# Kernel tuning notes

Hardware: AMD Instinct MI355X
Metric: run time of the kernel (lower is better)

## Reference

```python
import jax, jax.numpy as jnp
import numpy as np
import math

B, C, T0, Q0 = 2, 48, 250, 65
H = 192; KS = 4; HS = 1; NH = 4; E = 8; F = 65; DV = 12; HID2 = 384
EPS = 1e-5


def ln_clamp(x, g, b, axes, eps=EPS):
    # LayerNormalization4D / 4DCF: std = sqrt(clamp(var, eps))
    mu = x.mean(axis=axes, keepdims=True)
    var = x.var(axis=axes, keepdims=True)
    return (x - mu) / jnp.sqrt(jnp.maximum(var, eps)) * g + b


def torch_ln(x, g, b, eps=EPS):
    # torch.nn.LayerNorm over last dim: sqrt(var + eps)
    mu = x.mean(axis=-1, keepdims=True)
    var = x.var(axis=-1, keepdims=True)
    return (x - mu) / jnp.sqrt(var + eps) * g + b


def mha(x, in_w, in_b, out_w, out_b, nh):
    # torch.nn.MultiheadAttention, batch_first, self-attention
    N, L, Cm = x.shape
    qkv = x @ in_w.T + in_b
    q, k, v = jnp.split(qkv, 3, axis=-1)
    dh = Cm // nh
    hd = lambda t: t.reshape(N, L, nh, dh).transpose(0, 2, 1, 3)
    q, k, v = hd(q), hd(k), hd(v)
    att = jax.nn.softmax(jnp.einsum('nhld,nhmd->nhlm', q, k) / jnp.sqrt(jnp.float32(dh)), axis=-1)
    o = jnp.einsum('nhlm,nhmd->nhld', att, v).transpose(0, 2, 1, 3).reshape(N, L, Cm)
    return o @ out_w.T + out_b


def lstm_dir(x, wi, wh, bi, bh, reverse=False):
    # x: [N, L, D]; torch gate order i,f,g,o
    Hd = wh.shape[1]
    xs = jnp.swapaxes(x, 0, 1)
    if reverse:
        xs = xs[::-1]
    pre = jnp.einsum('lnd,gd->lng', xs, wi) + bi + bh  # [L,N,4H]

    def step(carry, p):
        hprev, cprev = carry
        gates = p + hprev @ wh.T
        i, f, g, o = jnp.split(gates, 4, axis=-1)
        c = jax.nn.sigmoid(f) * cprev + jax.nn.sigmoid(i) * jnp.tanh(g)
        hnew = jax.nn.sigmoid(o) * jnp.tanh(c)
        return (hnew, c), hnew

    h0 = jnp.zeros((x.shape[0], Hd), x.dtype)
    _, ys = jax.lax.scan(step, (h0, h0), pre)
    if reverse:
        ys = ys[::-1]
    return jnp.swapaxes(ys, 0, 1)


def bilstm(x, wif, whf, bif, bhf, wib, whb, bib, bhb):
    return jnp.concatenate([lstm_dir(x, wif, whf, bif, bhf, False),
                            lstm_dir(x, wib, whb, bib, bhb, True)], axis=-1)


def unfold1d(x, ks, hs):
    # x: [N, C, Q] -> [N, L, C*ks], channel-major like F.unfold
    N, Cc, Qq = x.shape
    L = (Qq - ks) // hs + 1
    cols = jnp.stack([x[:, :, k:k + (L - 1) * hs + 1:hs] for k in range(ks)], axis=-1)  # [N,C,L,ks]
    return cols.transpose(0, 2, 1, 3).reshape(N, L, Cc * ks)


def conv_transpose1d(x, w, b, stride):
    # x: [N, Cin, L], w: [Cin, Cout, ks] (torch ConvTranspose1d layout); overlap-add
    N, Ci, L = x.shape
    ks = w.shape[2]
    out_len = (L - 1) * stride + ks
    y = jnp.einsum('nil,iok->nolk', x, w)
    out = jnp.zeros((N, w.shape[1], out_len), x.dtype)
    for k in range(ks):
        out = out.at[:, :, k:k + (L - 1) * stride + 1:stride].add(y[..., k])
    return out + b[:, None]


def _forward(x, af_in_w, af_in_b, af_out_w, af_out_b, naf_g, naf_b, at_in_w, at_in_b, at_out_w, at_out_b, nat_g, nat_b, intra_ng, intra_nb, inter_ng, inter_nb, intra_wif, intra_whf, intra_bif, intra_bhf, intra_wib, intra_whb, intra_bib, intra_bhb, inter_wif, inter_whf, inter_bif, inter_bhf, inter_wib, inter_whb, inter_bib, inter_bhb, il_w, il_b, itl_w, itl_b, qw, qb, qa, qg, qbt, kw, kb, ka, kg, kbt, vw, vb, va, vg, vbt, pw, pb, pa, pg, pbt, fin_w, fin_b, fdw_w, fdw_b, fout_w, fout_b):
    Bb, Cc, old_T, old_Q = x.shape
    T = math.ceil((old_T - KS) / HS) * HS + KS
    Qd = math.ceil((old_Q - KS) / HS) * HS + KS
    x = jnp.pad(x, ((0, 0), (0, 0), (0, T - old_T), (0, Qd - old_Q)))
    input_ = x

    # ---- intra (frequency) path ----
    z = ln_clamp(input_, intra_ng[None, :, None, None], intra_nb[None, :, None, None], (1,))
    seq = z.transpose(0, 2, 3, 1).reshape(Bb * T, Qd, Cc)  # [B*T, Q, C]
    att = mha(seq, af_in_w, af_in_b, af_out_w, af_out_b, NH)
    seq = torch_ln(att + seq, naf_g, naf_b)
    u = unfold1d(seq.transpose(0, 2, 1), KS, HS)
    r = bilstm(u, intra_wif, intra_whf, intra_bif, intra_bhf, intra_wib, intra_whb, intra_bib, intra_bhb)
    r = conv_transpose1d(r.transpose(0, 2, 1), il_w, il_b, HS)  # [B*T, C, Qd]
    intra = r.reshape(Bb, T, Cc, Qd).transpose(0, 2, 1, 3) + input_
    input_ = intra

    # ---- inter (time) path ----
    z = ln_clamp(input_, inter_ng[None, :, None, None], inter_nb[None, :, None, None], (1,))
    seq = z.transpose(0, 3, 2, 1).reshape(Bb * Qd, T, Cc)  # [B*Q, T, C]
    att = mha(seq, at_in_w, at_in_b, at_out_w, at_out_b, NH)
    seq = torch_ln(att + seq, nat_g, nat_b)
    u = unfold1d(seq.transpose(0, 2, 1), KS, HS)
    r = bilstm(u, inter_wif, inter_whf, inter_bif, inter_bhf, inter_wib, inter_whb, inter_bib, inter_bhb)
    r = conv_transpose1d(r.transpose(0, 2, 1), itl_w, itl_b, HS)  # [B*Qd, C, T]
    inter = r.reshape(Bb, Qd, Cc, T).transpose(0, 2, 3, 1) + input_
    inter = inter[:, :, :old_T, :old_Q]

    # ---- custom per-head conv attention ----
    bt = inter  # [B, C, t, f]

    def head_proj(w, bias, a, g, beta):
        y = jnp.einsum('bctf,hec->hbetf', bt, w) + bias[:, None, :, None, None]
        y = jnp.where(y >= 0, y, a[:, None, None, None, None] * y)  # PReLU per head
        return ln_clamp(y, g[:, None, :, None, :], beta[:, None, :, None, :], (2, 4))

    Qh = head_proj(qw, qb, qa, qg, qbt)  # [h,B,E,t,f]
    Kh = head_proj(kw, kb, ka, kg, kbt)
    Vh = head_proj(vw, vb, va, vg, vbt)  # [h,B,dv,t,f]
    h_, _, E_, t_, f_ = Qh.shape
    dv = Vh.shape[2]
    Qf = Qh.transpose(0, 1, 3, 2, 4).reshape(h_, Bb, t_, E_ * f_)
    Kf = Kh.transpose(0, 1, 3, 2, 4).reshape(h_, Bb, t_, E_ * f_)
    Vf = Vh.transpose(0, 1, 3, 2, 4).reshape(h_, Bb, t_, dv * f_)
    attm = jax.nn.softmax(jnp.einsum('hbtd,hbsd->hbts', Qf, Kf) / jnp.sqrt(jnp.float32(E_ * f_)), axis=-1)
    Vo = jnp.einsum('hbts,hbsd->hbtd', attm, Vf).reshape(h_, Bb, t_, dv, f_)
    Vo = Vo.transpose(1, 0, 3, 2, 4).reshape(Bb, h_ * dv, t_, f_)  # head-major channel concat
    pj = jnp.einsum('bctf,oc->botf', Vo, pw) + pb[None, :, None, None]
    pj = jnp.where(pj >= 0, pj, pa * pj)
    pj = ln_clamp(pj, pg[None, :, None, :], pbt[None, :, None, :], (1, 3))
    out = pj + inter

    # ---- gated-dconv FFN ----
    pi = jnp.einsum('bctf,oc->botf', out, fin_w) + fin_b[None, :, None, None]
    dwc = jax.lax.conv_general_dilated(pi, fdw_w, (1, 1), ((1, 1), (1, 1)),
                                       dimension_numbers=('NCHW', 'OIHW', 'NCHW'),
                                       feature_group_count=fdw_w.shape[0]) + fdw_b[None, :, None, None]
    x1, x2 = jnp.split(dwc, 2, axis=1)
    ffn = jnp.einsum('bctf,oc->botf', jax.nn.gelu(x1, approximate=False) * x2, fout_w) + fout_b[None, :, None, None]
    return ffn + out


def setup_inputs() -> dict:
    key = jax.random.key(0)
    cnt = [0]

    def rn(shape, s=0.05):
        cnt[0] += 1
        return jax.random.normal(jax.random.fold_in(key, cnt[0]), shape, dtype=jnp.float32) * s

    z = lambda *s: jnp.zeros(s, jnp.float32)
    o = lambda *s: jnp.ones(s, jnp.float32)
    d = {}
    d['x'] = rn((B, C, T0, Q0), 1.0)
    for p in ['af', 'at']:
        d[p + '_in_w'] = rn((3 * C, C)); d[p + '_in_b'] = z(3 * C)
        d[p + '_out_w'] = rn((C, C)); d[p + '_out_b'] = z(C)
    d['naf_g'] = o(C); d['naf_b'] = z(C); d['nat_g'] = o(C); d['nat_b'] = z(C)
    d['intra_ng'] = o(C); d['intra_nb'] = z(C); d['inter_ng'] = o(C); d['inter_nb'] = z(C)
    for p in ['intra', 'inter']:
        for s in ['f', 'b']:
            d[p + '_wi' + s] = rn((4 * H, C * KS)); d[p + '_wh' + s] = rn((4 * H, H))
            d[p + '_bi' + s] = z(4 * H); d[p + '_bh' + s] = z(4 * H)
    d['il_w'] = rn((2 * H, C, KS)); d['il_b'] = z(C)
    d['itl_w'] = rn((2 * H, C, KS)); d['itl_b'] = z(C)
    for p, dim in [('q', E), ('k', E), ('v', DV)]:
        d[p + 'w'] = rn((NH, dim, C)); d[p + 'b'] = z(NH, dim)
        d[p + 'a'] = 0.25 * o(NH); d[p + 'g'] = o(NH, dim, F); d[p + 'bt'] = z(NH, dim, F)
    d['pw'] = rn((C, C)); d['pb'] = z(C); d['pa'] = 0.25 * o(1); d['pg'] = o(C, F); d['pbt'] = z(C, F)
    d['fin_w'] = rn((HID2, C)); d['fin_b'] = z(HID2)
    d['fdw_w'] = rn((HID2, 1, 3, 3)); d['fdw_b'] = z(HID2)
    d['fout_w'] = rn((C, HID2 // 2)); d['fout_b'] = z(C)
    return d


def reference(x, af_in_w, af_in_b, af_out_w, af_out_b, naf_g, naf_b, at_in_w, at_in_b, at_out_w, at_out_b, nat_g, nat_b, intra_ng, intra_nb, inter_ng, inter_nb, intra_wif, intra_whf, intra_bif, intra_bhf, intra_wib, intra_whb, intra_bib, intra_bhb, inter_wif, inter_whf, inter_bif, inter_bhf, inter_wib, inter_whb, inter_bib, inter_bhb, il_w, il_b, itl_w, itl_b, qw, qb, qa, qg, qbt, kw, kb, ka, kg, kbt, vw, vb, va, vg, vbt, pw, pb, pa, pg, pbt, fin_w, fin_b, fdw_w, fdw_b, fout_w, fout_b):
    return _forward(x, af_in_w, af_in_b, af_out_w, af_out_b, naf_g, naf_b, at_in_w, at_in_b, at_out_w, at_out_b, nat_g, nat_b, intra_ng, intra_nb, inter_ng, inter_nb, intra_wif, intra_whf, intra_bif, intra_bhf, intra_wib, intra_whb, intra_bib, intra_bhb, inter_wif, inter_whf, inter_bif, inter_bhf, inter_wib, inter_whb, inter_bib, inter_bhb, il_w, il_b, itl_w, itl_b, qw, qb, qa, qg, qbt, kw, kb, ka, kg, kbt, vw, vb, va, vg, vbt, pw, pb, pa, pg, pbt, fin_w, fin_b, fdw_w, fdw_b, fout_w, fout_b)
```

## Files before the change

### kernel.cpp

```cpp
#include <hip/hip_runtime.h>
#include <math.h>

#define EPSV 1e-5f

typedef _Float16 v2h __attribute__((ext_vector_type(2)));

__device__ __forceinline__ float sigf(float x){ return 1.0f/(1.0f+__expf(-x)); }
__device__ __forceinline__ float tanhf_(float x){
  float c = fminf(fmaxf(x,-10.f),10.f);
  float e = __expf(2.0f*c);
  return (e-1.0f)/(e+1.0f);
}

__device__ __forceinline__ void ldsbar(){
  asm volatile("s_waitcnt lgkmcnt(0)\n\ts_barrier" ::: "memory");
}

__device__ __forceinline__ float dot2u(unsigned int a, unsigned int b, float c){
#if __has_builtin(__builtin_amdgcn_fdot2)
  v2h av = __builtin_bit_cast(v2h, a);
  v2h bv = __builtin_bit_cast(v2h, b);
  return __builtin_amdgcn_fdot2(av, bv, c, false);
#else
  v2h av = __builtin_bit_cast(v2h, a);
  v2h bv = __builtin_bit_cast(v2h, b);
  return c + (float)av.x*(float)bv.x + (float)av.y*(float)bv.y;
#endif
}

__global__ void k_ln_chan(const float* __restrict__ src, float* __restrict__ dst,
                          const float* __restrict__ g, const float* __restrict__ bb, int mode){
  int i = blockIdx.x*blockDim.x + threadIdx.x;
  const int total = 2*250*65;
  if (i >= total) return;
  int q = i % 65; int t = (i/65) % 250; int b = i/(65*250);
  const float* p = src + (size_t)b*48*250*65 + (size_t)t*65 + q;
  float s=0.f, ss=0.f;
  for (int c=0;c<48;c++){ float v = p[(size_t)c*250*65]; s+=v; ss+=v*v; }
  float mu = s*(1.0f/48.0f);
  float var = ss*(1.0f/48.0f) - mu*mu;
  float rs = rsqrtf(fmaxf(var, EPSV));
  float* d = (mode==0) ? dst + ((size_t)(b*250+t)*65 + q)*48
                       : dst + ((size_t)(b*65+q)*250 + t)*48;
  for (int c=0;c<48;c++){ float v = p[(size_t)c*250*65]; d[c] = (v-mu)*rs*g[c] + bb[c]; }
}

__global__ __launch_bounds__(256) void k_mha2(
    const float* __restrict__ seq, const float* __restrict__ inw,
    const float* __restrict__ inb, float* __restrict__ att, int N, int L){
  __shared__ float shq[250*12];
  __shared__ float shk[250*12];
  __shared__ float shv[250*12];
  int n = blockIdx.x, h = blockIdx.y;
  for (int i = threadIdx.x; i < L*36; i += 256){
    int l = i/36, jj = i - (i/36)*36;
    int sect = jj/12, d = jj - sect*12;
    int j = sect*48 + h*12 + d;
    const float* srow = seq + ((size_t)n*L + l)*48;
    const float* wrow = inw + j*48;
    float acc = inb[j];
    for (int c=0;c<48;c++) acc += srow[c]*wrow[c];
    float* dst = (sect==0)?shq:(sect==1)?shk:shv;
    dst[l*12+d] = acc;
  }
  __syncthreads();
  const float scale = 0.28867513459481287f;
  for (int r = threadIdx.x; r < L; r += 256){
    const float4* q4 = (const float4*)(shq + r*12);
    float4 q0 = q4[0], q1 = q4[1], q2 = q4[2];
    float m = -1e30f, den = 0.0f;
    float4 o0 = make_float4(0,0,0,0), o1 = make_float4(0,0,0,0), o2 = make_float4(0,0,0,0);
    for (int j=0; j<L; j++){
      const float4* k4 = (const float4*)(shk + j*12);
      float4 k0 = k4[0], k1 = k4[1], k2 = k4[2];
      float s = q0.x*k0.x + q0.y*k0.y + q0.z*k0.z + q0.w*k0.w
              + q1.x*k1.x + q1.y*k1.y + q1.z*k1.z + q1.w*k1.w
              + q2.x*k2.x + q2.y*k2.y + q2.z*k2.z + q2.w*k2.w;
      s *= scale;
      if (s > m){
        float corr = __expf(m - s);
        den *= corr;
        o0.x*=corr; o0.y*=corr; o0.z*=corr; o0.w*=corr;
        o1.x*=corr; o1.y*=corr; o1.z*=corr; o1.w*=corr;
        o2.x*=corr; o2.y*=corr; o2.z*=corr; o2.w*=corr;
        m = s;
      }
      float e = __expf(s - m);
      den += e;
      const float4* v4 = (const float4*)(shv + j*12);
      float4 v0 = v4[0], v1 = v4[1], v2 = v4[2];
      o0.x += e*v0.x; o0.y += e*v0.y; o0.z += e*v0.z; o0.w += e*v0.w;
      o1.x += e*v1.x; o1.y += e*v1.y; o1.z += e*v1.z; o1.w += e*v1.w;
      o2.x += e*v2.x; o2.y += e*v2.y; o2.z += e*v2.z; o2.w += e*v2.w;
    }
    float inv = 1.0f/den;
    float* outp = att + ((size_t)n*L + r)*48 + h*12;
    outp[0]=o0.x*inv; outp[1]=o0.y*inv; outp[2]=o0.z*inv; outp[3]=o0.w*inv;
    outp[4]=o1.x*inv; outp[5]=o1.y*inv; outp[6]=o1.z*inv; outp[7]=o1.w*inv;
    outp[8]=o2.x*inv; outp[9]=o2.y*inv; outp[10]=o2.z*inv; outp[11]=o2.w*inv;
  }
}

__global__ void k_projres(const float* __restrict__ att, const float* __restrict__ seq,
                          const float* __restrict__ w, const float* __restrict__ bias,
                          float* __restrict__ dst, int NL){
  int i = blockIdx.x*blockDim.x + threadIdx.x;
  if (i >= NL*48) return;
  int o = i % 48; int nl = i/48;
  const float* ar = att + (size_t)nl*48;
  const float* wr = w + o*48;
  float acc = bias[o] + seq[i];
  for (int c=0;c<48;c++) acc += ar[c]*wr[c];
  dst[i] = acc;
}

__global__ void k_rowln(float* __restrict__ buf, const float* __restrict__ g,
                        const float* __restrict__ bb, int NL){
  int nl = blockIdx.x*blockDim.x + threadIdx.x;
  if (nl >= NL) return;
  float* p = buf + (size_t)nl*48;
  float s=0.f, ss=0.f;
  for (int c=0;c<48;c++){ float v=p[c]; s+=v; ss+=v*v; }
  float mu = s*(1.0f/48.0f);
  float var = ss*(1.0f/48.0f) - mu*mu;
  float rs = rsqrtf(var + EPSV);
  for (int c=0;c<48;c++) p[c] = (p[c]-mu)*rs*g[c] + bb[c];
}

__global__ void k_prep(const float* __restrict__ s0, const float* __restrict__ s1,
                       const float* __restrict__ s2, const float* __restrict__ s3,
                       const float* __restrict__ s4, const float* __restrict__ s5,
                       const float* __restrict__ s6, const float* __restrict__ s7,
                       const float* __restrict__ c0, const float* __restrict__ c1,
                       unsigned int* __restrict__ wpk, unsigned int* __restrict__ wtp){
  int i = blockIdx.x*blockDim.x + threadIdx.x;
  if (i < 589824){
    int seg = i/73728, off = i - seg*73728;
    const float* w = (seg==0)?s0:(seg==1)?s1:(seg==2)?s2:(seg==3)?s3:(seg==4)?s4:(seg==5)?s5:(seg==6)?s6:s7;
    int g = off % 768, d2 = off / 768;
    v2h v; v.x = (_Float16)w[g*192 + 2*d2]; v.y = (_Float16)w[g*192 + 2*d2 + 1];
    wpk[(size_t)seg*73728 + (size_t)d2*768 + g] = __builtin_bit_cast(unsigned int, v);
  } else if (i < 589824 + 2*36864){
    int j = i - 589824;
    int seg = j/36864, off = j - seg*36864;
    const float* w = seg ? c1 : c0;
    int c = off % 48; int ii2 = (off/48) % 192; int k = off/(48*192);
    v2h v;
    v.x = (_Float16)w[(2*ii2)*192 + c*4 + k];
    v.y = (_Float16)w[(2*ii2+1)*192 + c*4 + k];
    wtp[(size_t)seg*36864 + off] = __builtin_bit_cast(unsigned int, v);
  }
}

__global__ __launch_bounds__(256) void k_pregates(
    const float* __restrict__ seq2, const unsigned int* __restrict__ wi,
    const float* __restrict__ bi, const float* __restrict__ bh,
    _Float16* __restrict__ pre, int L2, int SL){
  __shared__ unsigned int ut[96*16];
  int n = blockIdx.y;
  int l0 = blockIdx.x*16;
  int t = threadIdx.x;
  for (int idx=t; idx<1536; idx+=256){
    int l = idx & 15, d2 = idx >> 4;
    int li = l0 + l;
    int c = d2 >> 1, k0 = (d2 & 1)*2;
    float u0=0.f, u1=0.f;
    if (li < L2){
      const float* p = seq2 + ((size_t)n*SL + li)*48;
      u0 = p[k0*48 + c];
      u1 = p[(k0+1)*48 + c];
    }
    v2h v; v.x=(_Float16)u0; v.y=(_Float16)u1;
    ut[d2*16 + l] = __builtin_bit_cast(unsigned int, v);
  }
  __syncthreads();
  float acc[3][16];
  float b0 = bi[t] + bh[t];
  float b1 = bi[t+256] + bh[t+256];
  float b2 = bi[t+512] + bh[t+512];
  #pragma unroll
  for (int l=0;l<16;l++){ acc[0][l]=b0; acc[1][l]=b1; acc[2][l]=b2; }
  #pragma unroll 4
  for (int d2=0; d2<96; d2++){
    unsigned int w0 = wi[(size_t)d2*768 + t];
    unsigned int w1 = wi[(size_t)d2*768 + t + 256];
    unsigned int w2 = wi[(size_t)d2*768 + t + 512];
    const uint4* u4 = (const uint4*)(ut + d2*16);
    #pragma unroll
    for (int l4=0; l4<4; l4++){
      uint4 uu = u4[l4];
      acc[0][l4*4+0] = dot2u(uu.x, w0, acc[0][l4*4+0]);
      acc[0][l4*4+1] = dot2u(uu.y, w0, acc[0][l4*4+1]);
      acc[0][l4*4+2] = dot2u(uu.z, w0, acc[0][l4*4+2]);
      acc[0][l4*4+3] = dot2u(uu.w, w0, acc[0][l4*4+3]);
      acc[1][l4*4+0] = dot2u(uu.x, w1, acc[1][l4*4+0]);
      acc[1][l4*4+1] = dot2u(uu.y, w1, acc[1][l4*4+1]);
      acc[1][l4*4+2] = dot2u(uu.z, w1, acc[1][l4*4+2]);
      acc[1][l4*4+3] = dot2u(uu.w, w1, acc[1][l4*4+3]);
      acc[2][l4*4+0] = dot2u(uu.x, w2, acc[2][l4*4+0]);
      acc[2][l4*4+1] = dot2u(uu.y, w2, acc[2][l4*4+1]);
      acc[2][l4*4+2] = dot2u(uu.z, w2, acc[2][l4*4+2]);
      acc[2][l4*4+3] = dot2u(uu.w, w2, acc[2][l4*4+3]);
    }
  }
  #pragma unroll
  for (int l=0;l<16;l++){
    int li = l0 + l;
    if (li < L2){
      _Float16* pr = pre + ((size_t)n*L2 + li)*768;
      pr[t]       = (_Float16)acc[0][l];
      pr[t+256]   = (_Float16)acc[1][l];
      pr[t+512]   = (_Float16)acc[2][l];
    }
  }
}

template<int G>
__global__ __launch_bounds__(1024) void k_lstm6(
    const _Float16* __restrict__ pre, unsigned int* __restrict__ rT2,
    const unsigned int* __restrict__ wh_f, const unsigned int* __restrict__ wh_b,
    int N, int L2){
  __shared__ unsigned int hh2[96*G];
  __shared__ float gpart[4*G*768];
  _Float16* hh2h = (_Float16*)hh2;
  int t = threadIdx.x;
  int q = t >> 8, tt = t & 255;
  int dir = blockIdx.y;
  int n0 = blockIdx.x*G;
  const unsigned int* wh = dir ? wh_b : wh_f;
  unsigned int wq[24][3];
  #pragma unroll
  for (int i=0;i<24;i++){
    const unsigned int* wr = wh + (size_t)(q*24+i)*768 + tt;
    wq[i][0] = wr[0]; wq[i][1] = wr[256]; wq[i][2] = wr[512];
  }
  const _Float16* prd = pre + (size_t)dir*(size_t)N*L2*768;
  float cst = 0.f;
  int as = t/192, aj = t - as*192;
  bool actv = (t < 192*G);
  const unsigned short* pbase = (const unsigned short*)prd;
  if (actv) pbase = (const unsigned short*)(prd + ((size_t)(n0+as)*L2)*768) + aj;
  for (int idx=t; idx<96*G; idx+=1024) hh2[idx]=0u;
  __syncthreads();

  unsigned short c0=0,c1=0,c2=0,c3=0;
  {
    int l0 = dir ? (L2-1) : 0;
    if (actv){
      const unsigned short* pp = pbase + (size_t)l0*768;
      c0 = pp[0]; c1 = pp[192]; c2 = pp[384]; c3 = pp[576];
    }
  }

  for (int step=0; step<L2; step++){
    int l = dir ? (L2-1-step) : step;
    int stepn = (step+1 < L2) ? (step+1) : step;
    int ln = dir ? (L2-1-stepn) : stepn;
    unsigned short pn0=0,pn1=0,pn2=0,pn3=0;
    if (actv){
      const unsigned short* pp = pbase + (size_t)ln*768;
      pn0 = pp[0]; pn1 = pp[192]; pn2 = pp[384]; pn3 = pp[576];
    }

    float acc0[G], acc1[G], acc2[G];
    #pragma unroll
    for (int s=0;s<G;s++){ acc0[s]=0.f; acc1[s]=0.f; acc2[s]=0.f; }
    #pragma unroll
    for (int i=0;i<24;i++){
      unsigned int hhv[G];
      if (G==4){
        uint4 hv = ((const uint4*)hh2)[q*24+i];
        hhv[0]=hv.x; hhv[1]=hv.y; hhv[2]=hv.z; hhv[3]=hv.w;
      } else if (G==2){
        uint2 hv = ((const uint2*)hh2)[q*24+i];
        hhv[0]=hv.x; hhv[1]=hv.y;
      } else {
        hhv[0] = hh2[q*24+i];
      }
      unsigned int w0 = wq[i][0], w1 = wq[i][1], w2 = wq[i][2];
      #pragma unroll
      for (int s=0;s<G;s++){
        acc0[s] = dot2u(hhv[s], w0, acc0[s]);
        acc1[s] = dot2u(hhv[s], w1, acc1[s]);
        acc2[s] = dot2u(hhv[s], w2, acc2[s]);
      }
    }
    #pragma unroll
    for (int s=0;s<G;s++){
      gpart[(q*G+s)*768 + tt]       = acc0[s];
      gpart[(q*G+s)*768 + tt + 256] = acc1[s];
      gpart[(q*G+s)*768 + tt + 512] = acc2[s];
    }
    ldsbar();

    if (actv){
      float gi = (float)__builtin_bit_cast(_Float16, c0);
      float gf = (float)__builtin_bit_cast(_Float16, c1);
      float gg = (float)__builtin_bit_cast(_Float16, c2);
      float go = (float)__builtin_bit_cast(_Float16, c3);
      #pragma unroll
      for (int qq=0; qq<4; qq++){
        const float* gp = gpart + (qq*G+as)*768;
        gi += gp[aj]; gf += gp[aj+192]; gg += gp[aj+384]; go += gp[aj+576];
      }
      float ig = sigf(gi), fg = sigf(gf), g2 = tanhf_(gg), og = sigf(go);
      cst = fg*cst + ig*g2;
      float hn = og*tanhf_(cst);
      hh2h[((aj>>1)*G + as)*2 + (aj&1)] = (_Float16)hn;
    }
    ldsbar();

    if (t < 96*G){
      int s = t/96, ii2 = t - s*96;
      unsigned int v = hh2[ii2*G + s];
      rT2[((size_t)(n0+s)*192 + dir*96 + ii2)*L2 + l] = v;
    }
    c0 = pn0; c1 = pn1; c2 = pn2; c3 = pn3;
  }
}

__global__ __launch_bounds__(256) void k_convt4(
    const unsigned int* __restrict__ rT2, const unsigned int* __restrict__ wtp,
    const float* __restrict__ bias, const float* __restrict__ resid,
    float* __restrict__ dst, int L2, int OL, int mode){
  int n = blockIdx.y;
  int pos = blockIdx.x*64 + (threadIdx.x & 63);
  int cq = __builtin_amdgcn_readfirstlane((int)(threadIdx.x >> 6));
  float acc[12];
  #pragma unroll
  for (int c=0;c<12;c++) acc[c]=0.f;
  const unsigned int* rbase = rT2 + (size_t)n*192*L2;
  for (int k=0;k<4;k++){
    int l = pos - k;
    bool v = (l>=0) && (l<L2);
    int lc = v ? l : 0;
    const unsigned int* wk = wtp + (size_t)k*192*48 + cq*12;
    #pragma unroll 4
    for (int ii2=0; ii2<192; ii2++){
      unsigned int rp = v ? rbase[(size_t)ii2*L2 + lc] : 0u;
      const unsigned int* wrow = wk + ii2*48;
      #pragma unroll
      for (int c=0;c<12;c++) acc[c] = dot2u(rp, wrow[c], acc[c]);
    }
  }
  if (pos < OL){
    for (int c12=0;c12<12;c12++){
      int c = cq*12 + c12;
      size_t oidx;
      if (mode==0){ int b=n/250, t=n%250; oidx = (((size_t)b*48+c)*250+t)*65+pos; }
      else        { int b=n/65,  qq=n%65; oidx = (((size_t)b*48+c)*250+pos)*65+qq; }
      dst[oidx] = acc[c12] + bias[c] + resid[oidx];
    }
  }
}

__global__ __launch_bounds__(256) void k_hproj(
    const float* __restrict__ bt, const float* __restrict__ w,
    const float* __restrict__ bias, const float* __restrict__ alpha,
    const float* __restrict__ g, const float* __restrict__ beta,
    float* __restrict__ dst, int dim, int kt_mode){
  __shared__ float tsh[3120];
  __shared__ float ybuf[780];
  __shared__ float r1[256];
  __shared__ float r2[256];
  int bx = blockIdx.x;
  int h = bx/500; int rem = bx - h*500; int b = rem/250; int t = rem - b*250;
  int ny = dim*65;
  int tid = threadIdx.x;
  const float* bbase = bt + (size_t)b*48*250*65 + (size_t)t*65;
  for (int kidx=tid; kidx<3120; kidx+=256){
    int c = kidx/65, f = kidx - c*65;
    tsh[kidx] = bbase[(size_t)c*250*65 + f];
  }
  __syncthreads();
  float al = alpha[h];
  float s=0.f, ss=0.f;
  for (int kidx=tid; kidx<ny; kidx+=256){
    int e = kidx/65, f = kidx - e*65;
    const float* wr = w + (h*dim+e)*48;
    float acc = bias[h*dim+e];
    for (int c=0;c<48;c++) acc += tsh[c*65+f]*wr[c];
    if (acc < 0.f) acc *= al;
    ybuf[kidx] = acc; s += acc; ss += acc*acc;
  }
  r1[tid]=s; r2[tid]=ss; __syncthreads();
  for (int st=128; st>0; st>>=1){
    if (tid<st){ r1[tid]+=r1[tid+st]; r2[tid]+=r2[tid+st]; }
    __syncthreads();
  }
  float mu = r1[0]/(float)ny, var = r2[0]/(float)ny - mu*mu;
  float rs = rsqrtf(fmaxf(var, EPSV));
  for (int kidx=tid; kidx<ny; kidx+=256){
    float y = (ybuf[kidx]-mu)*rs*g[h*ny+kidx] + beta[h*ny+kidx];
    if (kt_mode) dst[((size_t)(h*2+b)*520 + kidx)*250 + t] = y;
    else         dst[(size_t)bx*ny + kidx] = y;
  }
}

__global__ __launch_bounds__(256) void k_headattn2(
    const float* __restrict__ Qp, const float* __restrict__ KT,
    const float* __restrict__ Vp, float* __restrict__ Vo){
  __shared__ float qsh[10*520];
  __shared__ float psh[10*250];
  __shared__ float rinv[10];
  int t0 = blockIdx.x*10;
  int hb = blockIdx.y;
  int h = hb >> 1, b = hb & 1;
  int tid = threadIdx.x;
  const float* qbase = Qp + ((size_t)hb*250 + t0)*520;
  for (int i=tid; i<5200; i+=256) qsh[i] = qbase[i];
  __syncthreads();
  const float scale = 0.04385290096535147f;
  if (tid < 250){
    float sc[10];
    #pragma unroll
    for (int i=0;i<10;i++) sc[i]=0.f;
    const float* kcol = KT + (size_t)hb*520*250 + tid;
    for (int d=0; d<520; d++){
      float kv = kcol[(size_t)d*250];
      #pragma unroll
      for (int i=0;i<10;i++) sc[i] += qsh[i*520+d]*kv;
    }
    #pragma unroll
    for (int i=0;i<10;i++) psh[i*250+tid] = sc[i]*scale;
  }
  __syncthreads();
  if (tid < 10){
    float m = -1e30f;
    for (int s2=0;s2<250;s2++) m = fmaxf(m, psh[tid*250+s2]);
    float den = 0.f;
    for (int s2=0;s2<250;s2++){
      float e = __expf(psh[tid*250+s2]-m);
      psh[tid*250+s2]=e; den+=e;
    }
    rinv[tid] = 1.0f/den;
  }
  __syncthreads();
  float acc[10][4];
  #pragma unroll
  for (int i=0;i<10;i++)
    #pragma unroll
    for (int s=0;s<4;s++) acc[i][s]=0.f;
  for (int s2=0; s2<250; s2++){
    const float* vrow = Vp + ((size_t)hb*250 + s2)*780;
    float p[10];
    #pragma unroll
    for (int i=0;i<10;i++) p[i] = psh[i*250+s2];
    #pragma unroll
    for (int slot=0; slot<4; slot++){
      int d = tid + slot*256;
      if (d < 780){
        float v = vrow[d];
        #pragma unroll
        for (int i=0;i<10;i++) acc[i][slot] += p[i]*v;
      }
    }
  }
  #pragma unroll
  for (int slot=0; slot<4; slot++){
    int d = tid + slot*256;
    if (d < 780){
      int e = d/65, f = d - e*65;
      #pragma unroll
      for (int i=0;i<10;i++){
        Vo[(((size_t)b*48 + h*12 + e)*250 + (t0+i))*65 + f] = acc[i][slot]*rinv[i];
      }
    }
  }
}

__global__ __launch_bounds__(256) void k_pprojln(
    const float* __restrict__ Vo, const float* __restrict__ pw,
    const float* __restrict__ pb, const float* __restrict__ pa,
    const float* __restrict__ pg, const float* __restrict__ pbt,
    const float* __restrict__ inter, float* __restrict__ outb){
  __shared__ float vsh[3120];
  __shared__ float ysh[3120];
  __shared__ float r1[256];
  __shared__ float r2[256];
  int bx = blockIdx.x;
  int t = bx % 250, b = bx/250;
  int tid = threadIdx.x;
  const float* vbase = Vo + (size_t)b*48*250*65 + (size_t)t*65;
  for (int k=tid; k<3120; k+=256){
    int c = k/65, f = k - c*65;
    vsh[k] = vbase[(size_t)c*250*65 + f];
  }
  __syncthreads();
  float pav = pa[0];
  float s=0.f, ss=0.f;
  for (int k=tid; k<3120; k+=256){
    int o = k/65, f = k - o*65;
    const float* wr = pw + o*48;
    float acc = pb[o];
    for (int c=0;c<48;c++) acc += vsh[c*65+f]*wr[c];
    if (acc < 0.f) acc *= pav;
    ysh[k] = acc; s += acc; ss += acc*acc;
  }
  r1[tid]=s; r2[tid]=ss; __syncthreads();
  for (int st=128; st>0; st>>=1){
    if (tid<st){ r1[tid]+=r1[tid+st]; r2[tid]+=r2[tid+st]; }
    __syncthreads();
  }
  float mu = r1[0]*(1.0f/3120.0f), var = r2[0]*(1.0f/3120.0f) - mu*mu;
  float rs = rsqrtf(fmaxf(var, EPSV));
  for (int k=tid; k<3120; k+=256){
    int c = k/65, f = k - c*65;
    size_t idx = (((size_t)b*48+c)*250 + t)*65 + f;
    outb[idx] = (ysh[k]-mu)*rs*pg[k] + pbt[k] + inter[idx];
  }
}

__global__ void k_fin2(const float* __restrict__ outb, const float* __restrict__ w,
                       const float* __restrict__ bias, float* __restrict__ pi){
  int i = blockIdx.x*blockDim.x + threadIdx.x;
  if (i >= 2*96*250*65) return;
  int f = i % 65;
  int t = (i/65) % 250;
  int og = (i/(65*250)) % 96;
  int b = i/(65*250*96);
  const float* xp = outb + (size_t)b*48*250*65 + (size_t)t*65 + f;
  const float* w0 = w + og*4*48;
  float a0=bias[og*4], a1=bias[og*4+1], a2=bias[og*4+2], a3=bias[og*4+3];
  for (int c=0;c<48;c++){
    float xv = xp[(size_t)c*250*65];
    a0 += xv*w0[c]; a1 += xv*w0[48+c]; a2 += xv*w0[96+c]; a3 += xv*w0[144+c];
  }
  size_t o0 = (((size_t)b*384 + og*4)*250 + t)*65 + f;
  pi[o0] = a0; pi[o0+16250] = a1; pi[o0+2*16250] = a2; pi[o0+3*16250] = a3;
}

__global__ void k_dwg(const float* __restrict__ pi, const float* __restrict__ dw,
                      const float* __restrict__ db, float* __restrict__ gbuf){
  int i = blockIdx.x*blockDim.x + threadIdx.x;
  if (i >= 2*192*250*65) return;
  int f = i % 65;
  int t = (i/65) % 250;
  int j = (i/(65*250)) % 192;
  int b = i/(65*250*192);
  float x12[2];
  for (int half=0; half<2; half++){
    int ch = j + half*192;
    const float* base = pi + ((size_t)b*384 + ch)*250*65;
    const float* wr = dw + ch*9;
    float acc = db[ch];
    for (int dt=-1; dt<=1; dt++){
      int tt = t+dt;
      if (tt<0||tt>=250) continue;
      for (int df=-1; df<=1; df++){
        int ff = f+df;
        if (ff<0||ff>=65) continue;
        acc += base[(size_t)tt*65+ff]*wr[(dt+1)*3 + (df+1)];
      }
    }
    x12[half]=acc;
  }
  float x1 = x12[0];
  float g = 0.5f*x1*(1.0f+erff(x1*0.70710678118654752f));
  gbuf[i] = g * x12[1];
}

__global__ void k_final2(const float* __restrict__ gbuf, const float* __restrict__ w,
                         const float* __restrict__ bias, const float* __restrict__ outb,
                         float* __restrict__ dout){
  int i = blockIdx.x*blockDim.x + threadIdx.x;
  if (i >= 2*12*250*65) return;
  int f = i % 65;
  int t = (i/65) % 250;
  int og = (i/(65*250)) % 12;
  int b = i/(65*250*12);
  const float* gp = gbuf + (size_t)b*192*250*65 + (size_t)t*65 + f;
  const float* w0 = w + og*4*192;
  float a0=bias[og*4], a1=bias[og*4+1], a2=bias[og*4+2], a3=bias[og*4+3];
  for (int j=0;j<192;j++){
    float gv = gp[(size_t)j*250*65];
    a0 += gv*w0[j]; a1 += gv*w0[192+j]; a2 += gv*w0[384+j]; a3 += gv*w0[576+j];
  }
  size_t o0 = (((size_t)b*48 + og*4)*250 + t)*65 + f;
  dout[o0]         = a0 + outb[o0];
  dout[o0+16250]   = a1 + outb[o0+16250];
  dout[o0+2*16250] = a2 + outb[o0+2*16250];
  dout[o0+3*16250] = a3 + outb[o0+3*16250];
}

extern "C" void kernel_launch(void* const* d_in, const int* in_sizes, int n_in,
                              void* d_out, int out_size, void* d_ws, size_t ws_size,
                              hipStream_t stream) {
  (void)in_sizes; (void)n_in; (void)out_size; (void)ws_size;
  auto in = [&](int i){ return (const float*)d_in[i]; };
  const float* x        = in(0);
  const float* af_in_w  = in(1);  const float* af_in_b  = in(2);
  const float* af_out_w = in(3);  const float* af_out_b = in(4);
  const float* at_in_w  = in(5);  const float* at_in_b  = in(6);
  const float* at_out_w = in(7);  const float* at_out_b = in(8);
  const float* naf_g = in(9),  *naf_b = in(10), *nat_g = in(11), *nat_b = in(12);
  const float* intra_ng = in(13), *intra_nb = in(14), *inter_ng = in(15), *inter_nb = in(16);
  const float* intra_wif = in(17), *intra_whf = in(18), *intra_bif = in(19), *intra_bhf = in(20);
  const float* intra_wib = in(21), *intra_whb = in(22), *intra_bib = in(23), *intra_bhb = in(24);
  const float* inter_wif = in(25), *inter_whf = in(26), *inter_bif = in(27), *inter_bhf = in(28);
  const float* inter_wib = in(29), *inter_whb = in(30), *inter_bib = in(31), *inter_bhb = in(32);
  const float* il_w = in(33), *il_b = in(34), *itl_w = in(35), *itl_b = in(36);
  const float* qw = in(37), *qb = in(38), *qa = in(39), *qg = in(40), *qbt = in(41);
  const float* kw = in(42), *kb = in(43), *ka = in(44), *kg = in(45), *kbt = in(46);
  const float* vw = in(47), *vb = in(48), *va = in(49), *vg = in(50), *vbt = in(51);
  const float* pw = in(52), *pb = in(53), *pa = in(54), *pg = in(55), *pbt = in(56);
  const float* fin_w = in(57), *fin_b = in(58), *fdw_w = in(59), *fdw_b = in(60);
  const float* fout_w = in(61), *fout_b = in(62);

  float* ws = (float*)d_ws;
  float* buf_intra = ws + 0;
  float* buf_bt    = ws + 1560000;
  float* buf_out   = ws + 3120000;
  unsigned int* wpk = (unsigned int*)(ws + 4680000);
  unsigned int* wtp = (unsigned int*)(ws + 5269824);
  float* scr       = ws + 5343552;
  float* s_seq2 = scr;
  float* s_seq  = scr + 1560000;
  float* s_att  = scr + 3120000;
  _Float16* s_pre = (_Float16*)(scr + 4680000);
  unsigned int* s_rT2 = (unsigned int*)(scr + 29340480);
  float* s_Qh = scr;
  float* s_KT = scr + 1040000;
  float* s_Vh = scr + 2080000;
  float* s_Vo = scr + 3640000;
  float* s_pi = scr;
  float* s_g  = scr + 12480000;

  const int thr = 256;
  auto cdiv = [](int a, int b){ return (a+b-1)/b; };

  k_prep<<<cdiv(663552,thr),thr,0,stream>>>(
      intra_wif, intra_whf, intra_wib, intra_whb,
      inter_wif, inter_whf, inter_wib, inter_whb,
      il_w, itl_w, wpk, wtp);

  k_ln_chan<<<cdiv(2*250*65,thr), thr, 0, stream>>>(x, s_seq, intra_ng, intra_nb, 0);
  k_mha2<<<dim3(500,4), 256, 0, stream>>>(s_seq, af_in_w, af_in_b, s_att, 500, 65);
  k_projres<<<cdiv(500*65*48,thr), thr, 0, stream>>>(s_att, s_seq, af_out_w, af_out_b, s_seq2, 500*65);
  k_rowln<<<cdiv(32500,thr), thr, 0, stream>>>(s_seq2, naf_g, naf_b, 32500);
  {
    const size_t dstr = (size_t)500*62*768;
    k_pregates<<<dim3(4,500), 256, 0, stream>>>(s_seq2, wpk+0*73728, intra_bif, intra_bhf, s_pre,        62, 65);
    k_pregates<<<dim3(4,500), 256, 0, stream>>>(s_seq2, wpk+2*73728, intra_bib, intra_bhb, s_pre + dstr, 62, 65);
  }
  k_lstm6<2><<<dim3(250,2), 1024, 0, stream>>>(s_pre, s_rT2, wpk+1*73728, wpk+3*73728, 500, 62);
  k_convt4<<<dim3(2,500), 256, 0, stream>>>(s_rT2, wtp+0*36864, il_b, x, buf_intra, 62, 65, 0);

  k_ln_chan<<<cdiv(2*250*65,thr),thr,0,stream>>>(buf_intra, s_seq, inter_ng, inter_nb, 1);
  k_mha2<<<dim3(130,4), 256, 0, stream>>>(s_seq, at_in_w, at_in_b, s_att, 130, 250);
  k_projres<<<cdiv(130*250*48,thr),thr,0,stream>>>(s_att, s_seq, at_out_w, at_out_b, s_seq2, 130*250);
  k_rowln<<<cdiv(32500,thr),thr,0,stream>>>(s_seq2, nat_g, nat_b, 32500);
  {
    const size_t dstr = (size_t)130*247*768;
    k_pregates<<<dim3(16,130), 256, 0, stream>>>(s_seq2, wpk+4*73728, inter_bif, inter_bhf, s_pre,        247, 250);
    k_pregates<<<dim3(16,130), 256, 0, stream>>>(s_seq2, wpk+6*73728, inter_bib, inter_bhb, s_pre + dstr, 247, 250);
  }
  k_lstm6<1><<<dim3(130,2), 1024, 0, stream>>>(s_pre, s_rT2, wpk+5*73728, wpk+7*73728, 130, 247);
  k_convt4<<<dim3(4,130), 256, 0, stream>>>(s_rT2, wtp+1*36864, itl_b, buf_intra, buf_bt, 247, 250, 1);

  k_hproj<<<2000,256,0,stream>>>(buf_bt, qw, qb, qa, qg, qbt, s_Qh, 8, 0);
  k_hproj<<<2000,256,0,stream>>>(buf_bt, kw, kb, ka, kg, kbt, s_KT, 8, 1);
  k_hproj<<<2000,256,0,stream>>>(buf_bt, vw, vb, va, vg, vbt, s_Vh, 12, 0);
  k_headattn2<<<dim3(25,8), 256, 0, stream>>>(s_Qh, s_KT, s_Vh, s_Vo);
  k_pprojln<<<500,256,0,stream>>>(s_Vo, pw, pb, pa, pg, pbt, buf_bt, buf_out);

  k_fin2<<<cdiv(2*96*250*65,thr),thr,0,stream>>>(buf_out, fin_w, fin_b, s_pi);
  k_dwg<<<cdiv(2*192*250*65,thr),thr,0,stream>>>(s_pi, fdw_w, fdw_b, s_g);
  k_final2<<<cdiv(2*12*250*65,thr),thr,0,stream>>>(s_g, fout_w, fout_b, buf_out, (float*)d_out);
}
```

Baseline: 2.542 ms.

## Split LSTM recurrent weights between transposed LDS copy and global streaming

The recurrent LSTM kernel drops from 1024 to 512 threads per block. The first half of the hidden-weight matrix is copied into LDS once, transposed, so each thread can read contiguous uint4 chunks. The other half is reloaded from global memory on every time step. This removes the large per-thread register weight cache and halves the partial-sum buffer and its reduction, aiming to cut register pressure and barrier cost. The trade-off is global or L2 weight traffic inside the serial time loop, a large LDS footprint, and half the threads doing the dot products.

```diff
diff --git a/kernel.cpp b/kernel.cpp
--- a/kernel.cpp
+++ b/kernel.cpp
@@ -216,31 +216,32 @@
 }
 
 template<int G>
-__global__ __launch_bounds__(1024) void k_lstm6(
+__global__ __launch_bounds__(512,1) void k_lstm11(
     const _Float16* __restrict__ pre, unsigned int* __restrict__ rT2,
     const unsigned int* __restrict__ wh_f, const unsigned int* __restrict__ wh_b,
     int N, int L2){
+  __shared__ unsigned int wshT[48*768];
   __shared__ unsigned int hh2[96*G];
-  __shared__ float gpart[4*G*768];
+  __shared__ float gpart[2*G*768];
   _Float16* hh2h = (_Float16*)hh2;
   int t = threadIdx.x;
-  int q = t >> 8, tt = t & 255;
+  int hf = t >> 8, tt = t & 255;
   int dir = blockIdx.y;
   int n0 = blockIdx.x*G;
   const unsigned int* wh = dir ? wh_b : wh_f;
-  unsigned int wq[24][3];
-  #pragma unroll
-  for (int i=0;i<24;i++){
-    const unsigned int* wr = wh + (size_t)(q*24+i)*768 + tt;
-    wq[i][0] = wr[0]; wq[i][1] = wr[256]; wq[i][2] = wr[512];
-  }
+
+  for (int idx=t; idx<48*768; idx+=512){
+    int d2 = idx/768, row = idx - d2*768;
+    wshT[row*48 + d2] = wh[idx];
+  }
+  for (int idx=t; idx<96*G; idx+=512) hh2[idx]=0u;
+
   const _Float16* prd = pre + (size_t)dir*(size_t)N*L2*768;
   float cst = 0.f;
   int as = t/192, aj = t - as*192;
   bool actv = (t < 192*G);
   const unsigned short* pbase = (const unsigned short*)prd;
   if (actv) pbase = (const unsigned short*)(prd + ((size_t)(n0+as)*L2)*768) + aj;
-  for (int idx=t; idx<96*G; idx+=1024) hh2[idx]=0u;
   __syncthreads();
 
   unsigned short c0=0,c1=0,c2=0,c3=0;
@@ -251,6 +252,8 @@
       c0 = pp[0]; c1 = pp[192]; c2 = pp[384]; c3 = pp[576];
     }
   }
+
+  const unsigned int* wstr = wh + 48*768 + tt;
 
   for (int step=0; step<L2; step++){
     int l = dir ? (L2-1-step) : step;
@@ -265,31 +268,62 @@
     float acc0[G], acc1[G], acc2[G];
     #pragma unroll
     for (int s=0;s<G;s++){ acc0[s]=0.f; acc1[s]=0.f; acc2[s]=0.f; }
-    #pragma unroll
-    for (int i=0;i<24;i++){
-      unsigned int hhv[G];
-      if (G==4){
-        uint4 hv = ((const uint4*)hh2)[q*24+i];
-        hhv[0]=hv.x; hhv[1]=hv.y; hhv[2]=hv.z; hhv[3]=hv.w;
-      } else if (G==2){
-        uint2 hv = ((const uint2*)hh2)[q*24+i];
-        hhv[0]=hv.x; hhv[1]=hv.y;
-      } else {
-        hhv[0] = hh2[q*24+i];
+
+    if (hf==0){
+      const uint4* w0p = (const uint4*)(wshT + (size_t)tt*48);
+      const uint4* w1p = (const uint4*)(wshT + (size_t)(tt+256)*48);
+      const uint4* w2p = (const uint4*)(wshT + (size_t)(tt+512)*48);
+      #pragma unroll 4
+      for (int blk=0; blk<12; blk++){
+        unsigned int hw[4][G];
+        if (G==1){
+          uint4 hv = ((const uint4*)hh2)[blk];
+          hw[0][0]=hv.x; hw[1][0]=hv.y; hw[2][0]=hv.z; hw[3][0]=hv.w;
+        } else {
+          uint4 ha = ((const uint4*)hh2)[blk*2];
+          uint4 hb = ((const uint4*)hh2)[blk*2+1];
+          hw[0][0]=ha.x; hw[0][1]=ha.y; hw[1][0]=ha.z; hw[1][1]=ha.w;
+          hw[2][0]=hb.x; hw[2][1]=hb.y; hw[3][0]=hb.z; hw[3][1]=hb.w;
+        }
+        uint4 w0 = w0p[blk], w1 = w1p[blk], w2 = w2p[blk];
+        const unsigned int* w0a = (const unsigned int*)&w0;
+        const unsigned int* w1a = (const unsigned int*)&w1;
+        const unsigned int* w2a = (const unsigned int*)&w2;
+        #pragma unroll
+        for (int j=0;j<4;j++){
+          #pragma unroll
+          for (int s=0;s<G;s++){
+            acc0[s] = dot2u(hw[j][s], w0a[j], acc0[s]);
+            acc1[s] = dot2u(hw[j][s], w1a[j], acc1[s]);
+            acc2[s] = dot2u(hw[j][s], w2a[j], acc2[s]);
+          }
+        }
       }
-      unsigned int w0 = wq[i][0], w1 = wq[i][1], w2 = wq[i][2];
-      #pragma unroll
-      for (int s=0;s<G;s++){
-        acc0[s] = dot2u(hhv[s], w0, acc0[s]);
-        acc1[s] = dot2u(hhv[s], w1, acc1[s]);
-        acc2[s] = dot2u(hhv[s], w2, acc2[s]);
+    } else {
+      #pragma unroll 8
+      for (int i=0;i<48;i++){
+        unsigned int h2v[G];
+        if (G==1){ h2v[0] = hh2[48+i]; }
+        else {
+          uint2 hv = *(const uint2*)&hh2[(48+i)*2];
+          h2v[0]=hv.x; h2v[1]=hv.y;
+        }
+        unsigned int w0 = wstr[(size_t)i*768];
+        unsigned int w1 = wstr[(size_t)i*768 + 256];
+        unsigned int w2 = wstr[(size_t)i*768 + 512];
+        #pragma unroll
+        for (int s=0;s<G;s++){
+          acc0[s] = dot2u(h2v[s], w0, acc0[s]);
+          acc1[s] = dot2u(h2v[s], w1, acc1[s]);
+          acc2[s] = dot2u(h2v[s], w2, acc2[s]);
+        }
       }
     }
     #pragma unroll
     for (int s=0;s<G;s++){
-      gpart[(q*G+s)*768 + tt]       = acc0[s];
-      gpart[(q*G+s)*768 + tt + 256] = acc1[s];
-      gpart[(q*G+s)*768 + tt + 512] = acc2[s];
+      gpart[(hf*G+s)*768 + tt]       = acc0[s];
+      gpart[(hf*G+s)*768 + tt + 256] = acc1[s];
+      gpart[(hf*G+s)*768 + tt + 512] = acc2[s];
     }
     ldsbar();
 
@@ -299,8 +333,8 @@
       float gg = (float)__builtin_bit_cast(_Float16, c2);
       float go = (float)__builtin_bit_cast(_Float16, c3);
       #pragma unroll
-      for (int qq=0; qq<4; qq++){
-        const float* gp = gpart + (qq*G+as)*768;
+      for (int hh=0; hh<2; hh++){
+        const float* gp = gpart + (hh*G+as)*768;
         gi += gp[aj]; gf += gp[aj+192]; gg += gp[aj+384]; go += gp[aj+576];
       }
       float ig = sigf(gi), fg = sigf(gf), g2 = tanhf_(gg), og = sigf(go);
@@ -643,7 +677,7 @@
     k_pregates<<<dim3(4,500), 256, 0, stream>>>(s_seq2, wpk+0*73728, intra_bif, intra_bhf, s_pre,        62, 65);
     k_pregates<<<dim3(4,500), 256, 0, stream>>>(s_seq2, wpk+2*73728, intra_bib, intra_bhb, s_pre + dstr, 62, 65);
   }
-  k_lstm6<2><<<dim3(250,2), 1024, 0, stream>>>(s_pre, s_rT2, wpk+1*73728, wpk+3*73728, 500, 62);
+  k_lstm11<2><<<dim3(250,2), 512, 0, stream>>>(s_pre, s_rT2, wpk+1*73728, wpk+3*73728, 500, 62);
   k_convt4<<<dim3(2,500), 256, 0, stream>>>(s_rT2, wtp+0*36864, il_b, x, buf_intra, 62, 65, 0);
 
   k_ln_chan<<<cdiv(2*250*65,thr),thr,0,stream>>>(buf_intra, s_seq, inter_ng, inter_nb, 1);
@@ -655,7 +689,7 @@
     k_pregates<<<dim3(16,130), 256, 0, stream>>>(s_seq2, wpk+4*73728, inter_bif, inter_bhf, s_pre,        247, 250);
     k_pregates<<<dim3(16,130), 256, 0, stream>>>(s_seq2, wpk+6*73728, inter_bib, inter_bhb, s_pre + dstr, 247, 250);
   }
-  k_lstm6<1><<<dim3(130,2), 1024, 0, stream>>>(s_pre, s_rT2, wpk+5*73728, wpk+7*73728, 130, 247);
+  k_lstm11<1><<<dim3(130,2), 512, 0, stream>>>(s_pre, s_rT2, wpk+5*73728, wpk+7*73728, 130, 247);
   k_convt4<<<dim3(4,130), 256, 0, stream>>>(s_rT2, wtp+1*36864, itl_b, buf_intra, buf_bt, 247, 250, 1);
 
   k_hproj<<<2000,256,0,stream>>>(buf_bt, qw, qb, qa, qg, qbt, s_Qh, 8, 0);
```

Result: slower. 3.440 ms (+35.3%).
